# Performance work log

Measured on AMD Instinct MI355X. Metric: run time of the kernel, lower is better.

The kernel has to match this reference:

```python
import jax, jax.numpy as jnp
import numpy as np

LOG2 = float(np.log(2.0))

def ssp(x):
    # shifted softplus, the PhysNet-family activation: softplus(x) - ln(2)
    return jax.nn.softplus(x) - LOG2

def setup_inputs() -> dict:
    key = jax.random.key(0)
    k1, k2, k3, k4, k5 = jax.random.split(key, 5)
    N, E, D_EDGE, D_RBF = 50000, 640000, 128, 64
    vi = jax.random.normal(k1, (N, D_EDGE), dtype=jnp.float32)
    rbf = jax.random.uniform(k2, (E, D_RBF), dtype=jnp.float32)
    edge_index = jax.random.randint(k3, (2, E), 0, N, dtype=jnp.int64)
    # torch.nn.Linear params: y = x @ W.T + b, W ~ U(-1/sqrt(fan_in), 1/sqrt(fan_in))
    s1 = 1.0 / np.sqrt(D_RBF)
    s2 = 1.0 / np.sqrt(3 * D_EDGE)
    W_rbf = jax.random.uniform(k4, (D_EDGE, D_RBF), jnp.float32, -s1, s1)
    b_rbf = jnp.zeros((D_EDGE,), jnp.float32)
    W_cat = jax.random.uniform(k5, (D_EDGE, 3 * D_EDGE), jnp.float32, -s2, s2)
    b_cat = jnp.zeros((D_EDGE,), jnp.float32)
    return {"vi": vi, "rbf": rbf, "W_rbf": W_rbf, "b_rbf": b_rbf,
            "W_cat": W_cat, "b_cat": b_cat, "edge_index": edge_index}

def reference(vi, rbf, W_rbf, b_rbf, W_cat, b_cat, edge_index):
    # gather endpoint features per edge: [E, D]
    h_i = vi[edge_index[0], :]
    h_j = vi[edge_index[1], :]
    rbf_proj = rbf @ W_rbf.T + b_rbf              # [E, D]
    concat_msg = jnp.concatenate([rbf_proj, h_j, h_i], axis=-1)  # [E, 3D]
    m_ji = ssp(concat_msg @ W_cat.T + b_cat)      # [E, D]
    return m_ji
```

## Files before the change

kernel.cpp:

```cpp
#include <hip/hip_runtime.h>
#include <cmath>

#define D  128
#define DR 64
#define NB 32

typedef float fx4    __attribute__((ext_vector_type(4)));
typedef float f32x16 __attribute__((ext_vector_type(16)));
typedef short short8v __attribute__((ext_vector_type(8)));

__device__ __forceinline__ float ssp_f(float x) {
  float m = fmaxf(x, 0.0f);
  float t = __expf(-fabsf(x));
  return m + __logf(1.0f + t) - 0.69314718055994531f;
}

__device__ __forceinline__ short f2bf(float f) {
  unsigned u = __float_as_uint(f);
  u = (u + 0x7FFFu + ((u >> 16) & 1u)) >> 16;
  return (short)u;
}

__device__ __forceinline__ float bf2f(unsigned short h) {
  return __uint_as_float(((unsigned)h) << 16);
}

__global__ __launch_bounds__(256) void stage0_kernel(
    const float* __restrict__ W_rbf, const float* __restrict__ b_rbf,
    const float* __restrict__ W_cat, const float* __restrict__ b_cat,
    float* __restrict__ weff, unsigned short* __restrict__ weffh,
    float* __restrict__ beff, int write_bf16)
{
  int gid = blockIdx.x * 256 + threadIdx.x;
  if (gid < D * DR) {
    int o = gid >> 6;
    int r = gid & 63;
    float acc = 0.0f;
    #pragma unroll 8
    for (int d = 0; d < D; ++d)
      acc = fmaf(W_cat[o * 384 + d], W_rbf[d * DR + r], acc);
    weff[gid] = acc;
    if (write_bf16) weffh[gid] = (unsigned short)f2bf(acc);
  }
  if (gid < D) {
    float acc = b_cat[gid];
    #pragma unroll 8
    for (int d = 0; d < D; ++d)
      acc = fmaf(b_rbf[d], W_cat[gid * 384 + d], acc);
    beff[gid] = acc;
  }
}

__global__ __launch_bounds__(256) void stage1_kernel(
    const float* __restrict__ vi, const float* __restrict__ W_cat,
    unsigned short* __restrict__ PjH, unsigned short* __restrict__ PiH, int N)
{
  __shared__ float vrow[NB * D];
  int base = blockIdx.x * NB;
  int t = threadIdx.x;
  for (int idx = t * 4; idx < NB * D; idx += 1024) {
    int n = base + (idx >> 7);
    float4 v = make_float4(0.f, 0.f, 0.f, 0.f);
    if (n < N) v = *(const float4*)&vi[(long)n * D + (idx & 127)];
    *(float4*)&vrow[idx] = v;
  }
  __syncthreads();

  int o     = t & 127;
  int which = t >> 7;
  const float* w = W_cat + (long)o * 384 + 128 + which * 128;
  unsigned short* P = which ? PiH : PjH;

  float acc[NB];
  #pragma unroll
  for (int n = 0; n < NB; ++n) acc[n] = 0.0f;

  for (int dd = 0; dd < D; dd += 4) {
    float4 wv = *(const float4*)&w[dd];
    #pragma unroll
    for (int n = 0; n < NB; ++n) {
      float4 v = *(const float4*)&vrow[n * D + dd];
      acc[n] = fmaf(wv.x, v.x, acc[n]);
      acc[n] = fmaf(wv.y, v.y, acc[n]);
      acc[n] = fmaf(wv.z, v.z, acc[n]);
      acc[n] = fmaf(wv.w, v.w, acc[n]);
    }
  }
  #pragma unroll
  for (int n = 0; n < NB; ++n) {
    int nn = base + n;
    if (nn < N) P[(long)nn * D + o] = (unsigned short)f2bf(acc[n]);
  }
}

__global__ __launch_bounds__(256) void edge_mfma_kernel(
    const float* __restrict__ rbf, const int* __restrict__ eidx,
    const unsigned short* __restrict__ weffh, const float* __restrict__ beff,
    const unsigned short* __restrict__ PjH, const unsigned short* __restrict__ PiH,
    float* __restrict__ out, int E)
{
  const int t    = threadIdx.x;
  const int lane = t & 63;
  const int row  = lane & 31;
  const int half = lane >> 5;
  const long wid  = (long)blockIdx.x * 4 + (t >> 6);
  const long base = wid * 64;
  if (base >= (long)E) return;

  short8v B[4][4];
  #pragma unroll
  for (int ct = 0; ct < 4; ++ct) {
    #pragma unroll
    for (int ks = 0; ks < 4; ++ks)
      B[ct][ks] = *(const short8v*)&weffh[(ct * 32 + row) * DR + ks * 16 + half * 8];
  }
  float bias[4];
  #pragma unroll
  for (int ct = 0; ct < 4; ++ct) bias[ct] = beff[ct * 32 + row];

  #pragma unroll
  for (int tile = 0; tile < 2; ++tile) {
    const long tb = base + (long)tile * 32;
    if (tb >= (long)E) break;
    long er = tb + row; if (er > (long)E - 1) er = (long)E - 1;

    const float* arow = rbf + er * DR + half * 8;
    short8v A[4];
    #pragma unroll
    for (int ks = 0; ks < 4; ++ks) {
      fx4 lo = __builtin_nontemporal_load((const fx4*)&arow[ks * 16]);
      fx4 hi = __builtin_nontemporal_load((const fx4*)&arow[ks * 16 + 4]);
      short8v a;
      a[0] = f2bf(lo.x); a[1] = f2bf(lo.y); a[2] = f2bf(lo.z); a[3] = f2bf(lo.w);
      a[4] = f2bf(hi.x); a[5] = f2bf(hi.y); a[6] = f2bf(hi.z); a[7] = f2bf(hi.w);
      A[ks] = a;
    }

    const int iv = eidx[er];
    const int jv = eidx[(long)E + er];

    #pragma unroll
    for (int ct = 0; ct < 4; ++ct) {
      float gj[16], gi[16];
      #pragma unroll
      for (int reg = 0; reg < 16; ++reg) {
        const int erl = (reg & 3) + 8 * (reg >> 2) + 4 * half;
        const int j = __shfl(jv, erl);
        const int i = __shfl(iv, erl);
        gj[reg] = bf2f(PjH[(long)j * D + ct * 32 + row]);
        gi[reg] = bf2f(PiH[(long)i * D + ct * 32 + row]);
      }
      __builtin_amdgcn_sched_barrier(0);

      f32x16 acc = (f32x16)(0.0f);
      acc = __builtin_amdgcn_mfma_f32_32x32x16_bf16(A[0], B[ct][0], acc, 0, 0, 0);
      acc = __builtin_amdgcn_mfma_f32_32x32x16_bf16(A[1], B[ct][1], acc, 0, 0, 0);
      acc = __builtin_amdgcn_mfma_f32_32x32x16_bf16(A[2], B[ct][2], acc, 0, 0, 0);
      acc = __builtin_amdgcn_mfma_f32_32x32x16_bf16(A[3], B[ct][3], acc, 0, 0, 0);

      #pragma unroll
      for (int reg = 0; reg < 16; ++reg) {
        const int erl = (reg & 3) + 8 * (reg >> 2) + 4 * half;
        const long ge = tb + erl;
        const float v = ssp_f(acc[reg] + gj[reg] + gi[reg] + bias[ct]);
        if (ge < (long)E)
          __builtin_nontemporal_store(v, &out[ge * D + ct * 32 + row]);
      }
    }
  }
}

template<int K, int WS, int WOFF, bool GATHER, bool INIT, bool FINAL>
__global__ __launch_bounds__(256) void pass_kernel(
    const float* __restrict__ src, const int* __restrict__ gidx,
    const float* __restrict__ W, const float* __restrict__ beff,
    float* __restrict__ out, int E)
{
  int e = blockIdx.x * 256 + threadIdx.x;
  if (e >= E) return;
  long rowi = GATHER ? (long)gidx[e] : (long)e;

  float4 rv[K / 4];
  const float4* sp = (const float4*)(src + rowi * K);
  #pragma unroll
  for (int c = 0; c < K / 4; ++c) rv[c] = sp[c];

  float* orow = out + (long)e * D;
  for (int ob = 0; ob < D; ob += 4) {
    float acc[4];
    if (INIT) {
      float4 b4 = *(const float4*)&beff[ob];
      acc[0] = b4.x; acc[1] = b4.y; acc[2] = b4.z; acc[3] = b4.w;
    } else {
      float4 p4 = *(const float4*)&orow[ob];
      acc[0] = p4.x; acc[1] = p4.y; acc[2] = p4.z; acc[3] = p4.w;
    }
    #pragma unroll
    for (int k = 0; k < 4; ++k) {
      const float4* wv = (const float4*)&W[(long)(ob + k) * WS + WOFF];
      float a = acc[k];
      #pragma unroll
      for (int c = 0; c < K / 4; ++c) {
        float4 w4 = wv[c]; float4 r4 = rv[c];
        a = fmaf(w4.x, r4.x, a); a = fmaf(w4.y, r4.y, a);
        a = fmaf(w4.z, r4.z, a); a = fmaf(w4.w, r4.w, a);
      }
      acc[k] = a;
    }
    float4 o4;
    o4.x = FINAL ? ssp_f(acc[0]) : acc[0];
    o4.y = FINAL ? ssp_f(acc[1]) : acc[1];
    o4.z = FINAL ? ssp_f(acc[2]) : acc[2];
    o4.w = FINAL ? ssp_f(acc[3]) : acc[3];
    *(float4*)&orow[ob] = o4;
  }
}

extern "C" void kernel_launch(void* const* d_in, const int* in_sizes, int n_in,
                              void* d_out, int out_size, void* d_ws, size_t ws_size,
                              hipStream_t stream)
{
  const float* vi    = (const float*)d_in[0];
  const float* rbf   = (const float*)d_in[1];
  const float* W_rbf = (const float*)d_in[2];
  const float* b_rbf = (const float*)d_in[3];
  const float* W_cat = (const float*)d_in[4];
  const float* b_cat = (const float*)d_in[5];
  const int*   eidx  = (const int*)d_in[6];

  const int N = in_sizes[0] / D;
  const int E = in_sizes[6] / 2;
  float* out = (float*)d_out;

  float* ws   = (float*)d_ws;
  float* weff = ws;
  float* beff = ws + D * DR;
  unsigned short* weffh = (unsigned short*)(ws + 8448);
  unsigned short* PjH = (unsigned short*)(ws + 8448 + 4096);
  unsigned short* PiH = PjH + (size_t)N * D;
  size_t need = (8448 + 4096 + (size_t)N * 128) * sizeof(float);

  const int use_fast = (ws_size >= need && E >= 1);
  stage0_kernel<<<32, 256, 0, stream>>>(W_rbf, b_rbf, W_cat, b_cat,
                                        weff, weffh, beff, use_fast);

  if (use_fast) {
    stage1_kernel<<<(N + NB - 1) / NB, 256, 0, stream>>>(vi, W_cat, PjH, PiH, N);
    long waves = ((long)E + 63) / 64;
    int fblocks = (int)((waves + 3) / 4);
    edge_mfma_kernel<<<fblocks, 256, 0, stream>>>(rbf, eidx, weffh, beff,
                                                  PjH, PiH, out, E);
  } else {
    int eblocks = (E + 255) / 256;
    pass_kernel<DR, DR, 0,  false, true,  false><<<eblocks, 256, 0, stream>>>(rbf, nullptr,  weff,  beff, out, E);
    pass_kernel<D, 384, 128, true, false, false><<<eblocks, 256, 0, stream>>>(vi,  eidx + E, W_cat, beff, out, E);
    pass_kernel<D, 384, 256, true, false, true ><<<eblocks, 256, 0, stream>>>(vi,  eidx,     W_cat, beff, out, E);
  }
}
```

Before: 287.3 us.

## Transpose MFMA operands so each lane owns one edge row for vector gathers and stores

Swaps the MFMA operand roles so the weight matrix is the A operand and rbf is the B operand. The accumulator is then laid out with each lane holding consecutive output columns of a single edge. This removes the per-element shuffles of edge indices and the scalar 2-byte gathers, replacing them with 8-byte vector gathers of the bf16 projections and 16-byte vector stores. Weight fragments are now reloaded from global/L2 for every column tile instead of being held in registers, trading register pressure for extra cached loads. Output stores also change from nontemporal to regular stores.

```diff
diff --git a/kernel.cpp b/kernel.cpp
--- a/kernel.cpp
+++ b/kernel.cpp
@@ -8,6 +8,7 @@
 typedef float fx4    __attribute__((ext_vector_type(4)));
 typedef float f32x16 __attribute__((ext_vector_type(16)));
 typedef short short8v __attribute__((ext_vector_type(8)));
+typedef unsigned uix2 __attribute__((ext_vector_type(2)));
 
 __device__ __forceinline__ float ssp_f(float x) {
   float m = fmaxf(x, 0.0f);
@@ -19,10 +20,6 @@
   unsigned u = __float_as_uint(f);
   u = (u + 0x7FFFu + ((u >> 16) & 1u)) >> 16;
   return (short)u;
-}
-
-__device__ __forceinline__ float bf2f(unsigned short h) {
-  return __uint_as_float(((unsigned)h) << 16);
 }
 
 __global__ __launch_bounds__(256) void stage0_kernel(
@@ -101,70 +98,80 @@
 {
   const int t    = threadIdx.x;
   const int lane = t & 63;
-  const int row  = lane & 31;
+  const int col  = lane & 31;
   const int half = lane >> 5;
   const long wid  = (long)blockIdx.x * 4 + (t >> 6);
   const long base = wid * 64;
   if (base >= (long)E) return;
 
-  short8v B[4][4];
-  #pragma unroll
-  for (int ct = 0; ct < 4; ++ct) {
-    #pragma unroll
-    for (int ks = 0; ks < 4; ++ks)
-      B[ct][ks] = *(const short8v*)&weffh[(ct * 32 + row) * DR + ks * 16 + half * 8];
-  }
-  float bias[4];
-  #pragma unroll
-  for (int ct = 0; ct < 4; ++ct) bias[ct] = beff[ct * 32 + row];
+  const char* PjB = (const char*)PjH;
+  const char* PiB = (const char*)PiH;
+  char* outB = (char*)out;
 
   #pragma unroll
   for (int tile = 0; tile < 2; ++tile) {
     const long tb = base + (long)tile * 32;
     if (tb >= (long)E) break;
-    long er = tb + row; if (er > (long)E - 1) er = (long)E - 1;
-
-    const float* arow = rbf + er * DR + half * 8;
-    short8v A[4];
+    const long e = tb + col;
+    const bool oke = e < (long)E;
+    const long ec = oke ? e : (long)E - 1;
+
+    const float* arow = rbf + ec * DR + half * 8;
+    short8v Bf[4];
     #pragma unroll
     for (int ks = 0; ks < 4; ++ks) {
       fx4 lo = __builtin_nontemporal_load((const fx4*)&arow[ks * 16]);
       fx4 hi = __builtin_nontemporal_load((const fx4*)&arow[ks * 16 + 4]);
-      short8v a;
-      a[0] = f2bf(lo.x); a[1] = f2bf(lo.y); a[2] = f2bf(lo.z); a[3] = f2bf(lo.w);
-      a[4] = f2bf(hi.x); a[5] = f2bf(hi.y); a[6] = f2bf(hi.z); a[7] = f2bf(hi.w);
-      A[ks] = a;
-    }
-
-    const int iv = eidx[er];
-    const int jv = eidx[(long)E + er];
+      short8v b;
+      b[0] = f2bf(lo.x); b[1] = f2bf(lo.y); b[2] = f2bf(lo.z); b[3] = f2bf(lo.w);
+      b[4] = f2bf(hi.x); b[5] = f2bf(hi.y); b[6] = f2bf(hi.z); b[7] = f2bf(hi.w);
+      Bf[ks] = b;
+    }
+
+    const long jbase = (long)eidx[(long)E + ec] << 8;
+    const long ibase = (long)eidx[ec] << 8;
+    const long obase = e << 9;
 
     #pragma unroll
     for (int ct = 0; ct < 4; ++ct) {
-      float gj[16], gi[16];
-      #pragma unroll
-      for (int reg = 0; reg < 16; ++reg) {
-        const int erl = (reg & 3) + 8 * (reg >> 2) + 4 * half;
-        const int j = __shfl(jv, erl);
-        const int i = __shfl(iv, erl);
-        gj[reg] = bf2f(PjH[(long)j * D + ct * 32 + row]);
-        gi[reg] = bf2f(PiH[(long)i * D + ct * 32 + row]);
+      short8v Af[4];
+      #pragma unroll
+      for (int ks = 0; ks < 4; ++ks)
+        Af[ks] = *(const short8v*)&weffh[(ct * 32 + col) * DR + ks * 16 + half * 8];
+
+      uix2 gj[4], gi[4];
+      fx4 bq[4];
+      #pragma unroll
+      for (int qd = 0; qd < 4; ++qd) {
+        gj[qd] = *(const uix2*)(PjB + jbase + ct * 64 + qd * 16 + half * 8);
+        gi[qd] = *(const uix2*)(PiB + ibase + ct * 64 + qd * 16 + half * 8);
+        bq[qd] = *(const fx4*)&beff[ct * 32 + qd * 8 + half * 4];
       }
       __builtin_amdgcn_sched_barrier(0);
 
       f32x16 acc = (f32x16)(0.0f);
-      acc = __builtin_amdgcn_mfma_f32_32x32x16_bf16(A[0], B[ct][0], acc, 0, 0, 0);
-      acc = __builtin_amdgcn_mfma_f32_32x32x16_bf16(A[1], B[ct][1], acc, 0, 0, 0);
-      acc = __builtin_amdgcn_mfma_f32_32x32x16_bf16(A[2], B[ct][2], acc, 0, 0, 0);
-      acc = __builtin_amdgcn_mfma_f32_32x32x16_bf16(A[3], B[ct][3], acc, 0, 0, 0);
-
-      #pragma unroll
-      for (int reg = 0; reg < 16; ++reg) {
-        const int erl = (reg & 3) + 8 * (reg >> 2) + 4 * half;
-        const long ge = tb + erl;
-        const float v = ssp_f(acc[reg] + gj[reg] + gi[reg] + bias[ct]);
-        if (ge < (long)E)
-          __builtin_nontemporal_store(v, &out[ge * D + ct * 32 + row]);
+      acc = __builtin_amdgcn_mfma_f32_32x32x16_bf16(Af[0], Bf[0], acc, 0, 0, 0);
+      acc = __builtin_amdgcn_mfma_f32_32x32x16_bf16(Af[1], Bf[1], acc, 0, 0, 0);
+      acc = __builtin_amdgcn_mfma_f32_32x32x16_bf16(Af[2], Bf[2], acc, 0, 0, 0);
+      acc = __builtin_amdgcn_mfma_f32_32x32x16_bf16(Af[3], Bf[3], acc, 0, 0, 0);
+
+      #pragma unroll
+      for (int qd = 0; qd < 4; ++qd) {
+        const float j0 = __uint_as_float(gj[qd].x << 16);
+        const float j1 = __uint_as_float(gj[qd].x & 0xFFFF0000u);
+        const float j2 = __uint_as_float(gj[qd].y << 16);
+        const float j3 = __uint_as_float(gj[qd].y & 0xFFFF0000u);
+        const float i0 = __uint_as_float(gi[qd].x << 16);
+        const float i1 = __uint_as_float(gi[qd].x & 0xFFFF0000u);
+        const float i2 = __uint_as_float(gi[qd].y << 16);
+        const float i3 = __uint_as_float(gi[qd].y & 0xFFFF0000u);
+        fx4 v;
+        v.x = ssp_f(acc[qd * 4 + 0] + j0 + i0 + bq[qd].x);
+        v.y = ssp_f(acc[qd * 4 + 1] + j1 + i1 + bq[qd].y);
+        v.z = ssp_f(acc[qd * 4 + 2] + j2 + i2 + bq[qd].z);
+        v.w = ssp_f(acc[qd * 4 + 3] + j3 + i3 + bq[qd].w);
+        if (oke)
+          *(fx4*)(outB + obase + ct * 128 + qd * 32 + half * 16) = v;
       }
     }
   }
```

Measured after the change: 359.8 us. 25.2% more time.
